# Kernel tuning notes

Measured on AMD Instinct MI355X. Metric: run time of the kernel, lower is better.

The kernel has to match this reference:

```python
import jax, jax.numpy as jnp
import numpy as np


def _aperture(samples_per_side):
    # circular aperture samples on a samples_per_side x samples_per_side grid,
    # keeping only X^2 + Y^2 <= 1 (same as the torch meshgrid+mask in forward).
    lin = np.linspace(-1.0, 1.0, samples_per_side, dtype=np.float32)
    X, Y = np.meshgrid(lin, lin, indexing='ij')
    m = (X ** 2 + Y ** 2) <= 1.0
    return jnp.asarray(X[m]), jnp.asarray(Y[m])


def setup_inputs() -> dict:
    key = jax.random.key(0)
    k = jax.random.split(key, 6)
    B, L, C, H, W = 4, 1, 4, 1024, 1024
    images = jax.random.uniform(k[0], (B, L, C, H, W), jnp.float32)
    alphas = jax.random.uniform(k[1], (B, L, 1, H, W), jnp.float32)
    coffs = jax.random.uniform(k[2], (B, L, 1, H, W), jnp.float32)  # per-pixel disparity
    K = 10.0 + 20.0 * jax.random.uniform(k[3], (B, 1, 1, 1), jnp.float32)  # blur strength
    depth_focus = 0.3 + 0.4 * jax.random.uniform(k[4], (B, 1, 1, 1), jnp.float32)
    Eta = 1.0 + 4.0 * jax.random.uniform(k[5], (B, 1, 1, 1), jnp.float32)
    return {"images": images, "alphas": alphas, "coffs": coffs, "K": K,
            "depth_focus": depth_focus, "Eta": Eta, "samples_per_side": 17}


def _render(images, alphas, coffs, K, depth_focus, Eta, xs, ys):
    B, L, C, H, W = images.shape
    HW = H * W
    img = images[:, 0].reshape(B, C, HW)        # [B,4,HW]
    alpha = alphas[:, 0, 0].reshape(B, HW)      # [B,HW]
    coff = coffs[:, 0, 0].reshape(B, HW)        # [B,HW]
    Kb = K[:, 0, 0, 0][:, None]                 # [B,1]
    df = depth_focus[:, 0, 0, 0][:, None]
    eta = Eta[:, 0, 0, 0][:, None]
    r = Kb * (coff - df)                        # signed CoC radius (pixels), [B,HW]
    r_abs = jnp.abs(r)
    yy, xx = jnp.meshgrid(jnp.arange(H, dtype=jnp.float32),
                          jnp.arange(W, dtype=jnp.float32), indexing='ij')
    xx = xx.reshape(HW)
    yy = yy.reshape(HW)

    def step(carry, s):
        xs_s, ys_s = s
        # gather source pixel along the aperture-sample direction, scaled by CoC
        sx = jnp.clip(jnp.round(xx[None, :] + r * xs_s), 0, W - 1).astype(jnp.int32)
        sy = jnp.clip(jnp.round(yy[None, :] + r * ys_s), 0, H - 1).astype(jnp.int32)
        idx = sy * W + sx                                        # [B,HW]
        img_q = jnp.take_along_axis(img, idx[:, None, :], axis=2)  # [B,4,HW]
        a_q = jnp.take_along_axis(alpha, idx, axis=1)              # [B,HW]
        r_q = jnp.take_along_axis(r_abs, idx, axis=1)               # [B,HW]
        dist = r_abs * jnp.sqrt(xs_s * xs_s + ys_s * ys_s)          # sample distance
        # soft test that the source CoC covers this pixel + energy normalization 1/(pi r^2)
        w = a_q * jax.nn.sigmoid(eta * (r_q - dist) + 1.0) / (jnp.pi * r_q * r_q + 1.0)
        bok, wc = carry
        return (bok + w[:, None, :] * img_q, wc + w), None

    init = (jnp.zeros((B, C, HW), jnp.float32), jnp.zeros((B, HW), jnp.float32))
    (bok, wc), _ = jax.lax.scan(step, init, (xs, ys))
    return bok.reshape(B, C, H, W), wc.reshape(B, 1, H, W)


def reference(images, alphas, coffs, K, depth_focus, Eta, samples_per_side):
    xs, ys = _aperture(samples_per_side)
    return _render(images, alphas, coffs, K, depth_focus, Eta, xs, ys)
```

## Files before the change

kernel.cpp:

```cpp
#include <hip/hip_runtime.h>
#include <hip/hip_fp16.h>
#include <math.h>

#define PI_F    3.14159274101257324f
#define LOG2E_F 1.4426950408889634f

#define TS_X   64
#define TS_Y   8
#define APRON  21
#define A_W    (TS_X + 2*APRON)
#define A_H    (TS_Y + 2*APRON)
#define ROWBYTES (A_W * 8)

extern "C" __global__ void __launch_bounds__(256)
dof_prepass8(const float* __restrict__ img, const float* __restrict__ alpha,
             const float* __restrict__ coff, const float* __restrict__ Kp,
             const float* __restrict__ dfp, const float* __restrict__ etap,
             uint2* __restrict__ R, int HW, int B)
{
    int t = blockIdx.x * blockDim.x + threadIdx.x;
    int quads = (B * HW) >> 2;
    if (t >= quads) return;
    int tid4 = t << 2;
    int b = tid4 / HW;
    int p = tid4 - b * HW;
    float kb = Kp[b], dfb = dfp[b], etab = etap[b];

    float4 cf = *(const float4*)(coff + tid4);
    float4 al = *(const float4*)(alpha + tid4);
    const float* ib = img + (size_t)b * 4 * HW + p;
    float4 c0 = *(const float4*)(ib);
    float4 c1 = *(const float4*)(ib + (size_t)HW);
    float4 c2 = *(const float4*)(ib + (size_t)2 * HW);
    float4 c3 = *(const float4*)(ib + (size_t)3 * HW);

    const float cfa[4] = {cf.x, cf.y, cf.z, cf.w};
    const float ala[4] = {al.x, al.y, al.z, al.w};
    const float v0a[4] = {c0.x, c0.y, c0.z, c0.w};
    const float v1a[4] = {c1.x, c1.y, c1.z, c1.w};
    const float v2a[4] = {c2.x, c2.y, c2.z, c2.w};
    const float v3a[4] = {c3.x, c3.y, c3.z, c3.w};

    unsigned rec[8];
#pragma unroll
    for (int u = 0; u < 4; ++u) {
        float r  = kb * (cfa[u] - dfb);
        float ra = fabsf(r);
        float denom = fmaf(PI_F * ra, ra, 1.0f);
        float amp = ala[u] * __builtin_amdgcn_rcpf(denom);
        float EL  = fmaf(etab, ra, 1.0f) * LOG2E_F;
        unsigned q0 = (unsigned)rintf(fminf(v0a[u] * amp, 1.0f) * 255.0f);
        unsigned q1 = (unsigned)rintf(fminf(v1a[u] * amp, 1.0f) * 255.0f);
        unsigned q2 = (unsigned)rintf(fminf(v2a[u] * amp, 1.0f) * 255.0f);
        unsigned q3 = (unsigned)rintf(fminf(v3a[u] * amp, 1.0f) * 255.0f);
        __half2 h = __halves2half2(__float2half_rn(amp), __float2half_rn(EL));
        rec[2*u]   = q0 | (q1 << 8) | (q2 << 16) | (q3 << 24);
        rec[2*u+1] = __builtin_bit_cast(unsigned, h);
    }
    uint4* Ro = (uint4*)(R + tid4);
    Ro[0] = make_uint4(rec[0], rec[1], rec[2], rec[3]);
    Ro[1] = make_uint4(rec[4], rec[5], rec[6], rec[7]);
}

extern "C" __global__ void __launch_bounds__(512, 6)
dof_render8_lds(const uint2* __restrict__ R,
                const float* __restrict__ coff, const float* __restrict__ Kp,
                const float* __restrict__ dfp, const float* __restrict__ etap,
                const int* __restrict__ sps, float* __restrict__ out, int B)
{
    const int HW = 1024 * 1024;
    const float INV255 = 0.00392156862745098f;

    __shared__ uint2 tile[A_H * A_W];

    int x0 = blockIdx.x << 6;
    int y0 = blockIdx.y << 3;
    int b  = blockIdx.z;
    int ax0 = x0 - APRON;
    int ay0 = y0 - APRON;

    const uint2* Rb = R + (size_t)b * HW;
    for (int k = threadIdx.x; k < A_H * A_W; k += 512) {
        int iy = k / A_W;
        int ix = k - iy * A_W;
        int gx = ax0 + ix; gx = gx < 0 ? 0 : (gx > 1023 ? 1023 : gx);
        int gy = ay0 + iy; gy = gy < 0 ? 0 : (gy > 1023 ? 1023 : gy);
        tile[k] = Rb[(gy << 10) + gx];
    }
    __syncthreads();

    int tx = threadIdx.x & 63;
    int ty = threadIdx.x >> 6;
    int x = x0 + tx, y = y0 + ty;
    int p = (y << 10) + x;
    int tid = (b << 20) + p;

    float kb = Kp[b], dfb = dfp[b], etab = etap[b];
    float r  = kb * (coff[tid] - dfb);
    float ra = fabsf(r);
    float ernL = etab * ra * LOG2E_F;
    float xf = (float)x, yf = (float)y;

    float a0 = 0.f, a1 = 0.f, a2 = 0.f, a3 = 0.f, aw = 0.f;
    const char* tbase = (const char*)tile;

    if (sps[0] == 17) {
        float rx[17];
#pragma unroll
        for (int i = 0; i < 17; ++i)
            rx[i] = __fmul_rn(ra, (float)i * 0.125f - 1.0f);

        int sxo[17], rowb[17];
#pragma unroll
        for (int i = 0; i < 17; ++i) {
            int sx = (int)rintf(__fadd_rn(xf, rx[i]));
            sxo[i] = (sx - ax0) << 3;
            int sy = (int)rintf(__fadd_rn(yf, rx[i]));
            rowb[i] = (sy - ay0) * ROWBYTES;
        }

#pragma unroll
        for (int j = 0; j < 17; ++j) {
            const float ysv = (float)j * 0.125f - 1.0f;
            const float ys2 = ysv * ysv;
            const int rbase = rowb[j];
#pragma unroll
            for (int i = 0; i < 17; ++i) {
                const float xsv = (float)i * 0.125f - 1.0f;
                const float n2 = xsv * xsv + ys2;
                if (n2 <= 1.0f) {
                    const float norm = sqrtf(n2);
                    uint2 v = *(const uint2*)(tbase + rbase + sxo[i]);
                    float fq0 = (float)(v.x & 0xffu);
                    float fq1 = (float)((v.x >> 8) & 0xffu);
                    float fq2 = (float)((v.x >> 16) & 0xffu);
                    float fq3 = (float)(v.x >> 24);
                    __half2 hv = __builtin_bit_cast(__half2, v.y);
                    float ampq = __low2float(hv);
                    float ELq  = __high2float(hv);
                    float t = fmaf(ernL, norm, -ELq);
                    float s = __builtin_amdgcn_rcpf(1.0f + __builtin_amdgcn_exp2f(t));
                    a0 = fmaf(s, fq0, a0);
                    a1 = fmaf(s, fq1, a1);
                    a2 = fmaf(s, fq2, a2);
                    a3 = fmaf(s, fq3, a3);
                    aw = fmaf(s, ampq, aw);
                }
            }
        }
        a0 *= INV255; a1 *= INV255; a2 *= INV255; a3 *= INV255;
    } else {
        int S = sps[0];
        float stepv = 2.0f / (float)(S - 1);
        for (int j = 0; j < S; ++j) {
            float ysv = fmaf((float)j, stepv, -1.0f);
            float ys2 = ysv * ysv;
            int sy = (int)rintf(__fadd_rn(yf, __fmul_rn(ra, ysv)));
            sy = sy < 0 ? 0 : (sy > 1023 ? 1023 : sy);
            int rowbyte = ((sy - ay0) * A_W - ax0) * 8;
            for (int i = 0; i < S; ++i) {
                float xsv = fmaf((float)i, stepv, -1.0f);
                float n2 = fmaf(xsv, xsv, ys2);
                if (n2 <= 1.0f) {
                    int sx = (int)rintf(__fadd_rn(xf, __fmul_rn(ra, xsv)));
                    sx = sx < 0 ? 0 : (sx > 1023 ? 1023 : sx);
                    uint2 v = *(const uint2*)(tbase + rowbyte + (sx << 3));
                    float fq0 = (float)(v.x & 0xffu);
                    float fq1 = (float)((v.x >> 8) & 0xffu);
                    float fq2 = (float)((v.x >> 16) & 0xffu);
                    float fq3 = (float)(v.x >> 24);
                    __half2 hv = __builtin_bit_cast(__half2, v.y);
                    float ampq = __low2float(hv);
                    float ELq  = __high2float(hv);
                    float t = fmaf(ernL, __builtin_amdgcn_sqrtf(n2), -ELq);
                    float s = __builtin_amdgcn_rcpf(1.0f + __builtin_amdgcn_exp2f(t));
                    float s255 = s * INV255;
                    a0 = fmaf(s255, fq0, a0);
                    a1 = fmaf(s255, fq1, a1);
                    a2 = fmaf(s255, fq2, a2);
                    a3 = fmaf(s255, fq3, a3);
                    aw = fmaf(s, ampq, aw);
                }
            }
        }
    }

    size_t obase = (size_t)b * 4 * HW + p;
    out[obase]                = a0;
    out[obase + (size_t)HW]   = a1;
    out[obase + (size_t)2*HW] = a2;
    out[obase + (size_t)3*HW] = a3;
    out[(size_t)B * 4 * HW + tid] = aw;
}

extern "C" __global__ void __launch_bounds__(256)
dof_render_direct(const float* __restrict__ img, const float* __restrict__ alpha,
                  const float* __restrict__ coff, const float* __restrict__ Kp,
                  const float* __restrict__ dfp, const float* __restrict__ etap,
                  const int* __restrict__ sps, float* __restrict__ out,
                  int H, int W, int B)
{
    int HW = H * W;
    int tid = blockIdx.x * blockDim.x + threadIdx.x;
    if (tid >= B * HW) return;
    int b = tid / HW;
    int p = tid - b * HW;
    int y = p / W;
    int x = p - y * W;

    float kb = Kp[b], dfb = dfp[b], etab = etap[b];
    float r  = kb * (coff[tid] - dfb);
    float ra = fabsf(r);

    int S = sps[0];
    float stepv = 2.0f / (float)(S - 1);

    const float* imgb   = img   + (size_t)b * 4 * HW;
    const float* alphab = alpha + (size_t)b * HW;
    const float* coffb  = coff  + (size_t)b * HW;
    float xf = (float)x, yf = (float)y;

    float a0 = 0.f, a1 = 0.f, a2 = 0.f, a3 = 0.f, aw = 0.f;

    for (int j = 0; j < S; ++j) {
        float ysv = fmaf((float)j, stepv, -1.0f);
        float ys2 = ysv * ysv;
        int sy = (int)rintf(__fadd_rn(yf, __fmul_rn(ra, ysv)));
        sy = sy < 0 ? 0 : (sy > H - 1 ? H - 1 : sy);
        int rowb = sy * W;
        for (int i = 0; i < S; ++i) {
            float xsv = fmaf((float)i, stepv, -1.0f);
            float n2 = fmaf(xsv, xsv, ys2);
            if (n2 <= 1.0f) {
                int sx = (int)rintf(__fadd_rn(xf, __fmul_rn(ra, xsv)));
                sx = sx < 0 ? 0 : (sx > W - 1 ? W - 1 : sx);
                int idx = rowb + sx;
                float aq = alphab[idx];
                float rq = fabsf(kb * (coffb[idx] - dfb));
                float dist = ra * __builtin_amdgcn_sqrtf(n2);
                float arg = fmaf(etab, rq - dist, 1.0f);
                float e = __builtin_amdgcn_exp2f(-arg * LOG2E_F);
                float s = __builtin_amdgcn_rcpf(1.0f + e);
                float w = aq * s * __builtin_amdgcn_rcpf(fmaf(PI_F * rq, rq, 1.0f));
                a0 = fmaf(w, imgb[idx], a0);
                a1 = fmaf(w, imgb[(size_t)HW + idx], a1);
                a2 = fmaf(w, imgb[(size_t)2*HW + idx], a2);
                a3 = fmaf(w, imgb[(size_t)3*HW + idx], a3);
                aw += w;
            }
        }
    }

    size_t obase = (size_t)b * 4 * HW + p;
    out[obase]                = a0;
    out[obase + (size_t)HW]   = a1;
    out[obase + (size_t)2*HW] = a2;
    out[obase + (size_t)3*HW] = a3;
    out[(size_t)B * 4 * HW + tid] = aw;
}

extern "C" void kernel_launch(void* const* d_in, const int* in_sizes, int n_in,
                              void* d_out, int out_size, void* d_ws, size_t ws_size,
                              hipStream_t stream) {
    const float* images = (const float*)d_in[0];
    const float* alphas = (const float*)d_in[1];
    const float* coffs  = (const float*)d_in[2];
    const float* Kp     = (const float*)d_in[3];
    const float* dfp    = (const float*)d_in[4];
    const float* etap   = (const float*)d_in[5];
    const int*   sps    = (const int*)d_in[6];

    int B  = in_sizes[3];
    int HW = in_sizes[1] / B;
    int W  = 1024;
    int H  = HW / W;

    float* out = (float*)d_out;
    int total = B * HW;

    size_t need8 = (size_t)total * sizeof(uint2);

    if (ws_size >= need8 && H == 1024 && W == 1024) {
        uint2* R = (uint2*)d_ws;
        int quads = total >> 2;
        dim3 blk(256), grd((quads + 255) / 256);
        dof_prepass8<<<grd, blk, 0, stream>>>(images, alphas, coffs, Kp, dfp,
                                              etap, R, HW, B);
        dim3 blk2(512), grd2(1024 / TS_X, 1024 / TS_Y, B);
        dof_render8_lds<<<grd2, blk2, 0, stream>>>(R, coffs, Kp, dfp, etap, sps,
                                                   out, B);
    } else {
        dim3 blk(256), grd((total + 255) / 256);
        dof_render_direct<<<grd, blk, 0, stream>>>(images, alphas, coffs, Kp, dfp,
                                                   etap, sps, out, H, W, B);
    }
}
```

Before: 476.5 us.

## Add fp16 packed prepass and 32x16-tile LDS render with specialized 17-sample loop

Adds a new prepass that stores per-pixel colour premultiplied by amplitude as four fp16 values, plus a separate fp16 pair of amplitude and sigmoid bias. A new render kernel uses 32x16 tiles with a 21-pixel apron in LDS and a fully unrolled path for 17 samples per side with precomputed offsets, falling back to a generic loop otherwise. The intent is to cut per-sample arithmetic in the sigmoid weight and reduce the LDS halo footprint per output pixel, with occupancy hinted through launch bounds. The cost is fp16 rounding of premultiplied colours and a larger workspace requirement.

```diff
diff --git a/kernel.cpp b/kernel.cpp
--- a/kernel.cpp
+++ b/kernel.cpp
@@ -5,12 +5,202 @@
 #define PI_F    3.14159274101257324f
 #define LOG2E_F 1.4426950408889634f
 
+#define APRON  21
+
 #define TS_X   64
 #define TS_Y   8
-#define APRON  21
 #define A_W    (TS_X + 2*APRON)
 #define A_H    (TS_Y + 2*APRON)
 #define ROWBYTES (A_W * 8)
+
+#define B_TSX  32
+#define B_TSY  16
+#define B_AW   (B_TSX + 2*APRON)
+#define B_AH   (B_TSY + 2*APRON)
+#define B_N    (B_AH * B_AW)
+#define B_ROWB (B_AW * 8)
+
+extern "C" __global__ void __launch_bounds__(256)
+dof_prepass16(const float* __restrict__ img, const float* __restrict__ alpha,
+              const float* __restrict__ coff, const float* __restrict__ Kp,
+              const float* __restrict__ dfp, const float* __restrict__ etap,
+              uint2* __restrict__ Rch, unsigned* __restrict__ Rae, int HW, int B)
+{
+    int t = blockIdx.x * blockDim.x + threadIdx.x;
+    int quads = (B * HW) >> 2;
+    if (t >= quads) return;
+    int tid4 = t << 2;
+    int b = tid4 / HW;
+    int p = tid4 - b * HW;
+    float kb = Kp[b], dfb = dfp[b], etab = etap[b];
+
+    float4 cf = *(const float4*)(coff + tid4);
+    float4 al = *(const float4*)(alpha + tid4);
+    const float* ib = img + (size_t)b * 4 * HW + p;
+    float4 c0 = *(const float4*)(ib);
+    float4 c1 = *(const float4*)(ib + (size_t)HW);
+    float4 c2 = *(const float4*)(ib + (size_t)2 * HW);
+    float4 c3 = *(const float4*)(ib + (size_t)3 * HW);
+
+    const float cfa[4] = {cf.x, cf.y, cf.z, cf.w};
+    const float ala[4] = {al.x, al.y, al.z, al.w};
+    const float v0a[4] = {c0.x, c0.y, c0.z, c0.w};
+    const float v1a[4] = {c1.x, c1.y, c1.z, c1.w};
+    const float v2a[4] = {c2.x, c2.y, c2.z, c2.w};
+    const float v3a[4] = {c3.x, c3.y, c3.z, c3.w};
+
+    unsigned ch[8];
+    unsigned ae[4];
+#pragma unroll
+    for (int u = 0; u < 4; ++u) {
+        float r  = kb * (cfa[u] - dfb);
+        float ra = fabsf(r);
+        float denom = fmaf(PI_F * ra, ra, 1.0f);
+        float amp = ala[u] * __builtin_amdgcn_rcpf(denom);
+        float EL  = fmaf(etab, ra, 1.0f) * LOG2E_F;
+        __half2 h01 = __halves2half2(__float2half_rn(v0a[u] * amp),
+                                     __float2half_rn(v1a[u] * amp));
+        __half2 h23 = __halves2half2(__float2half_rn(v2a[u] * amp),
+                                     __float2half_rn(v3a[u] * amp));
+        __half2 hae = __halves2half2(__float2half_rn(amp), __float2half_rn(EL));
+        ch[2*u]   = __builtin_bit_cast(unsigned, h01);
+        ch[2*u+1] = __builtin_bit_cast(unsigned, h23);
+        ae[u]     = __builtin_bit_cast(unsigned, hae);
+    }
+    uint4* Co = (uint4*)(Rch + tid4);
+    Co[0] = make_uint4(ch[0], ch[1], ch[2], ch[3]);
+    Co[1] = make_uint4(ch[4], ch[5], ch[6], ch[7]);
+    *(uint4*)(Rae + tid4) = make_uint4(ae[0], ae[1], ae[2], ae[3]);
+}
+
+extern "C" __global__ void __launch_bounds__(512, 6)
+dof_render16_lds(const uint2* __restrict__ Rch, const unsigned* __restrict__ Rae,
+                 const float* __restrict__ coff, const float* __restrict__ Kp,
+                 const float* __restrict__ dfp, const float* __restrict__ etap,
+                 const int* __restrict__ sps, float* __restrict__ out, int B)
+{
+    const int HW = 1024 * 1024;
+
+    __shared__ uint2    tCH[B_N];
+    __shared__ unsigned tAE[B_N];
+
+    int x0 = blockIdx.x << 5;
+    int y0 = blockIdx.y << 4;
+    int b  = blockIdx.z;
+    int ax0 = x0 - APRON;
+    int ay0 = y0 - APRON;
+
+    const uint2*    Cb = Rch + (size_t)b * HW;
+    const unsigned* Ab = Rae + (size_t)b * HW;
+    for (int k = threadIdx.x; k < B_N; k += 512) {
+        int iy = k / B_AW;
+        int ix = k - iy * B_AW;
+        int gx = ax0 + ix; gx = gx < 0 ? 0 : (gx > 1023 ? 1023 : gx);
+        int gy = ay0 + iy; gy = gy < 0 ? 0 : (gy > 1023 ? 1023 : gy);
+        int g = (gy << 10) + gx;
+        tCH[k] = Cb[g];
+        tAE[k] = Ab[g];
+    }
+    __syncthreads();
+
+    int tx = threadIdx.x & 31;
+    int ty = threadIdx.x >> 5;
+    int x = x0 + tx, y = y0 + ty;
+    int p = (y << 10) + x;
+    int tid = (b << 20) + p;
+
+    float kb = Kp[b], dfb = dfp[b], etab = etap[b];
+    float r  = kb * (coff[tid] - dfb);
+    float ra = fabsf(r);
+    float ernL = etab * ra * LOG2E_F;
+    float xf = (float)x, yf = (float)y;
+
+    float a0 = 0.f, a1 = 0.f, a2 = 0.f, a3 = 0.f, aw = 0.f;
+    const char* cbase = (const char*)tCH;
+    const char* abase = (const char*)tAE;
+
+    if (sps[0] == 17) {
+        float rx[17];
+#pragma unroll
+        for (int i = 0; i < 17; ++i)
+            rx[i] = __fmul_rn(ra, (float)i * 0.125f - 1.0f);
+
+        int sxo8[17], rowb8[17];
+#pragma unroll
+        for (int i = 0; i < 17; ++i) {
+            int sx = (int)rintf(__fadd_rn(xf, rx[i]));
+            sxo8[i] = (sx - ax0) << 3;
+            int sy = (int)rintf(__fadd_rn(yf, rx[i]));
+            rowb8[i] = (sy - ay0) * B_ROWB;
+        }
+
+#pragma unroll
+        for (int j = 0; j < 17; ++j) {
+            const float ysv = (float)j * 0.125f - 1.0f;
+            const float ys2 = ysv * ysv;
+            const int rbase = rowb8[j];
+#pragma unroll
+            for (int i = 0; i < 17; ++i) {
+                const float xsv = (float)i * 0.125f - 1.0f;
+                const float n2 = xsv * xsv + ys2;
+                if (n2 <= 1.0f) {
+                    const float norm = sqrtf(n2);
+                    int o8 = rbase + sxo8[i];
+                    uint2 vch = *(const uint2*)(cbase + o8);
+                    unsigned vae = *(const unsigned*)(abase + (o8 >> 1));
+                    __half2 h01 = __builtin_bit_cast(__half2, vch.x);
+                    __half2 h23 = __builtin_bit_cast(__half2, vch.y);
+                    __half2 hae = __builtin_bit_cast(__half2, vae);
+                    float t = fmaf(ernL, norm, -__high2float(hae));
+                    float s = __builtin_amdgcn_rcpf(1.0f + __builtin_amdgcn_exp2f(t));
+                    a0 = fmaf(s, __low2float(h01),  a0);
+                    a1 = fmaf(s, __high2float(h01), a1);
+                    a2 = fmaf(s, __low2float(h23),  a2);
+                    a3 = fmaf(s, __high2float(h23), a3);
+                    aw = fmaf(s, __low2float(hae),  aw);
+                }
+            }
+        }
+    } else {
+        int S = sps[0];
+        float stepv = 2.0f / (float)(S - 1);
+        for (int j = 0; j < S; ++j) {
+            float ysv = fmaf((float)j, stepv, -1.0f);
+            float ys2 = ysv * ysv;
+            int sy = (int)rintf(__fadd_rn(yf, __fmul_rn(ra, ysv)));
+            sy = sy < 0 ? 0 : (sy > 1023 ? 1023 : sy);
+            int rowbyte = ((sy - ay0) * B_AW - ax0) * 8;
+            for (int i = 0; i < S; ++i) {
+                float xsv = fmaf((float)i, stepv, -1.0f);
+                float n2 = fmaf(xsv, xsv, ys2);
+                if (n2 <= 1.0f) {
+                    int sx = (int)rintf(__fadd_rn(xf, __fmul_rn(ra, xsv)));
+                    sx = sx < 0 ? 0 : (sx > 1023 ? 1023 : sx);
+                    int o8 = rowbyte + (sx << 3);
+                    uint2 vch = *(const uint2*)(cbase + o8);
+                    unsigned vae = *(const unsigned*)(abase + (o8 >> 1));
+                    __half2 h01 = __builtin_bit_cast(__half2, vch.x);
+                    __half2 h23 = __builtin_bit_cast(__half2, vch.y);
+                    __half2 hae = __builtin_bit_cast(__half2, vae);
+                    float t = fmaf(ernL, __builtin_amdgcn_sqrtf(n2), -__high2float(hae));
+                    float s = __builtin_amdgcn_rcpf(1.0f + __builtin_amdgcn_exp2f(t));
+                    a0 = fmaf(s, __low2float(h01),  a0);
+                    a1 = fmaf(s, __high2float(h01), a1);
+                    a2 = fmaf(s, __low2float(h23),  a2);
+                    a3 = fmaf(s, __high2float(h23), a3);
+                    aw = fmaf(s, __low2float(hae),  aw);
+                }
+            }
+        }
+    }
+
+    size_t obase = (size_t)b * 4 * HW + p;
+    out[obase]                = a0;
+    out[obase + (size_t)HW]   = a1;
+    out[obase + (size_t)2*HW] = a2;
+    out[obase + (size_t)3*HW] = a3;
+    out[(size_t)B * 4 * HW + tid] = aw;
+}
 
 extern "C" __global__ void __launch_bounds__(256)
 dof_prepass8(const float* __restrict__ img, const float* __restrict__ alpha,
@@ -278,9 +468,20 @@
     float* out = (float*)d_out;
     int total = B * HW;
 
-    size_t need8 = (size_t)total * sizeof(uint2);
-
-    if (ws_size >= need8 && H == 1024 && W == 1024) {
+    size_t need16 = (size_t)total * 12;
+    size_t need8  = (size_t)total * sizeof(uint2);
+
+    if (ws_size >= need16 && H == 1024 && W == 1024) {
+        uint2*    Rch = (uint2*)d_ws;
+        unsigned* Rae = (unsigned*)((char*)d_ws + (size_t)total * 8);
+        int quads = total >> 2;
+        dim3 blk(256), grd((quads + 255) / 256);
+        dof_prepass16<<<grd, blk, 0, stream>>>(images, alphas, coffs, Kp, dfp,
+                                               etap, Rch, Rae, HW, B);
+        dim3 blk2(512), grd2(1024 / B_TSX, 1024 / B_TSY, B);
+        dof_render16_lds<<<grd2, blk2, 0, stream>>>(Rch, Rae, coffs, Kp, dfp,
+                                                    etap, sps, out, B);
+    } else if (ws_size >= need8 && H == 1024 && W == 1024) {
         uint2* R = (uint2*)d_ws;
         int quads = total >> 2;
         dim3 blk(256), grd((quads + 255) / 256);
```

Measured after the change: 504.9 us. 6.0% more time.
